# Optimization experiments

Measured on AMD Instinct MI355X. Metric: run time of the kernel, lower is better.

The kernel has to match this reference:

```python
import jax, jax.numpy as jnp
import numpy as np

DIM = 512
HID = 1024        # dim * expansion_factor
QK = 128          # query_key_dim
G = 256           # group_size
EPS = 1e-5


def setup_inputs() -> dict:
    key = jax.random.key(0)
    ks = jax.random.split(key, 6)
    x = jax.random.normal(ks[0], (4, 4096, DIM), jnp.float32)
    ln_w = jnp.ones((DIM,), jnp.float32)
    ln_b = jnp.zeros((DIM,), jnp.float32)
    Wh = 0.02 * jax.random.normal(ks[1], (DIM, 2 * HID), jnp.float32)
    bh = jnp.zeros((2 * HID,), jnp.float32)
    Wqk = 0.02 * jax.random.normal(ks[2], (DIM, QK), jnp.float32)
    bqk = jnp.zeros((QK,), jnp.float32)
    gamma = 0.02 * jax.random.normal(ks[3], (4, QK), jnp.float32)  # nn.init.normal_(gamma, std=0.02)
    beta = jnp.zeros((4, QK), jnp.float32)
    Wo = 0.02 * jax.random.normal(ks[4], (HID, DIM), jnp.float32)
    bo = jnp.zeros((DIM,), jnp.float32)
    return {"x": x, "ln_w": ln_w, "ln_b": ln_b, "Wh": Wh, "bh": bh,
            "Wqk": Wqk, "bqk": bqk, "gamma": gamma, "beta": beta,
            "Wo": Wo, "bo": bo}


def reference(x, ln_w, ln_b, Wh, bh, Wqk, bqk, gamma, beta, Wo, bo):
    b, n, _ = x.shape
    g = n // G  # number of groups (n chosen as multiple of G -> no padding)

    # LayerNorm (torch uses biased variance)
    mu = jnp.mean(x, axis=-1, keepdims=True)
    var = jnp.mean((x - mu) ** 2, axis=-1, keepdims=True)
    normed = (x - mu) * jax.lax.rsqrt(var + EPS) * ln_w + ln_b

    # to_hidden: Linear -> SiLU, split into v / gate
    h = jax.nn.silu(normed @ Wh + bh)            # [b, n, 2*HID]
    v, gate = jnp.split(h, 2, axis=-1)           # each [b, n, HID]

    # to_qk: Linear -> SiLU, then 4-head offset/scale
    qk = jax.nn.silu(normed @ Wqk + bqk)         # [b, n, QK]
    qkh = qk[..., None, :] * gamma + beta        # [b, n, 4, QK]
    quad_q, lin_q, quad_k, lin_k = (qkh[..., i, :] for i in range(4))

    # group: b (g n) d -> b g n d
    grp = lambda t: t.reshape(b, g, G, t.shape[-1])
    qq, qk_, lq, lk, vv = map(grp, (quad_q, quad_k, lin_q, lin_k, v))

    # quadratic (group-local) attention with ReLU^2 scores, causal within group
    sim = jnp.einsum('bgid,bgjd->bgij', qq, qk_) / G
    attn = jnp.square(jnp.maximum(sim, 0.0))
    causal_mask = jnp.triu(jnp.ones((G, G), dtype=bool), 1)
    attn = jnp.where(causal_mask, 0.0, attn)
    quad_out = jnp.einsum('bgij,bgje->bgie', attn, vv)   # [b, g, G, HID]

    # linear attention across groups: per-group kv, exclusive cumsum over group dim
    lin_kv = jnp.einsum('bgnd,bgne->bgde', lk, vv) / G   # [b, g, QK, HID]
    lin_kv = jnp.cumsum(lin_kv, axis=1)
    lin_kv = jnp.pad(lin_kv, ((0, 0), (1, 0), (0, 0), (0, 0)))[:, :-1]
    lin_out = jnp.einsum('bgde,bgnd->bgne', lin_kv, lq)  # [b, g, G, HID]

    out = gate * (quad_out.reshape(b, n, HID) + lin_out.reshape(b, n, HID))
    return out @ Wo + bo + x
```

## Files before the change

kernel.cpp:

```cpp
#include <hip/hip_runtime.h>
#include <hip/hip_bf16.h>
#include <math.h>


#define BATCH 4
#define SEQ   4096
#define TROWS 16384
#define DIMD  512
#define HIDD  1024
#define QKD   128
#define GRP   256
#define NGRP  16
#define BGRP  64
#define EPIW  132
#define EPB   130

typedef unsigned short bfraw;
typedef __attribute__((ext_vector_type(8))) short bf16x8;
typedef __attribute__((ext_vector_type(8))) unsigned short u16x8;
typedef __attribute__((ext_vector_type(4))) unsigned int u32x4;
typedef __attribute__((ext_vector_type(4))) float f32x4;

__device__ __forceinline__ float bf2f(bfraw u) {
    union { float f; unsigned int i; } c;
    c.i = ((unsigned int)u) << 16;
    return c.f;
}
__device__ __forceinline__ bfraw f2bf(float f) {
    unsigned int x = __float_as_uint(f);
    unsigned int r = (x + 0x7fffu + ((x >> 16) & 1u)) >> 16;
    return (bfraw)r;
}
__device__ __forceinline__ unsigned int pkbf(float lo, float hi) {
    __hip_bfloat162 h2 = __float22bfloat162_rn(make_float2(lo, hi));
    union { __hip_bfloat162 h; unsigned int u; } c; c.h = h2;
    return c.u;
}
__device__ __forceinline__ void store16bf(bfraw* dst, const float* src) {
    u32x4 a, b;
    #pragma unroll
    for (int k = 0; k < 4; ++k) a[k] = pkbf(src[2 * k], src[2 * k + 1]);
    #pragma unroll
    for (int k = 0; k < 4; ++k) b[k] = pkbf(src[8 + 2 * k], src[8 + 2 * k + 1]);
    *(u32x4*)dst = a;
    *(u32x4*)(dst + 8) = b;
}
__device__ __forceinline__ float silu_f(float z) {
    return z / (1.f + __expf(-z));
}
__device__ __forceinline__ void gload_lds16(const void* g, void* l) {
    __builtin_amdgcn_global_load_lds(
        (const __attribute__((address_space(1))) unsigned int*)g,
        (__attribute__((address_space(3))) unsigned int*)l, 16, 0, 0);
}

__device__ __forceinline__ void mfma_step(const bfraw* As, const bfraw* Bs,
                                          f32x4 acc[4][4], int wm, int wn,
                                          int q, int mi) {
    bf16x8 af[4], bfg[4];
    #pragma unroll
    for (int i = 0; i < 4; ++i)
        af[i] = *(const bf16x8*)&As[(size_t)(wm * 64 + i * 16 + mi) * 32 + q * 8];
    #pragma unroll
    for (int j = 0; j < 4; ++j)
        bfg[j] = *(const bf16x8*)&Bs[(size_t)(wn * 64 + j * 16 + mi) * 32 + q * 8];
    #pragma unroll
    for (int i = 0; i < 4; ++i)
        #pragma unroll
        for (int j = 0; j < 4; ++j)
            acc[i][j] = __builtin_amdgcn_mfma_f32_16x16x32_bf16(af[i], bfg[j], acc[i][j], 0, 0, 0);
}

#define SMEM_DECL(sz)                                           \
    __shared__ __align__(16) char smem_[sz];                    \
    bfraw* As0 = (bfraw*)smem_;                                 \
    bfraw* As1 = (bfraw*)(smem_ + 8192);                        \
    bfraw* Bs0 = (bfraw*)(smem_ + 16384);                       \
    bfraw* Bs1 = (bfraw*)(smem_ + 24576);

#define KLOOP_PRE(Abase, Astr, Bbase, Bstr)                                    \
    const bfraw* pa0 = (Abase) + (size_t)(t >> 2) * (Astr) + (t & 3) * 8;      \
    const bfraw* pa1 = pa0 + (size_t)64 * (Astr);                              \
    const bfraw* pb0 = (Bbase) + (size_t)(t >> 2) * (Bstr) + (t & 3) * 8;      \
    const bfraw* pb1 = pb0 + (size_t)64 * (Bstr);

#define LDS_DSTS                                                               \
    bfraw* lA0  = As0 + (size_t)wid * 512;                                     \
    bfraw* lA0b = As0 + 2048 + (size_t)wid * 512;                              \
    bfraw* lA1  = As1 + (size_t)wid * 512;                                     \
    bfraw* lA1b = As1 + 2048 + (size_t)wid * 512;                              \
    bfraw* lB0  = Bs0 + (size_t)wid * 512;                                     \
    bfraw* lB0b = Bs0 + 2048 + (size_t)wid * 512;                              \
    bfraw* lB1  = Bs1 + (size_t)wid * 512;                                     \
    bfraw* lB1b = Bs1 + 2048 + (size_t)wid * 512;

#define KSTEP64P                                                               \
    do {                                                                       \
        gload_lds16(pa0,      lA0);                                            \
        gload_lds16(pa1,      lA0b);                                           \
        gload_lds16(pa0 + 32, lA1);                                            \
        gload_lds16(pa1 + 32, lA1b);                                           \
        gload_lds16(pb0,      lB0);                                            \
        gload_lds16(pb1,      lB0b);                                           \
        gload_lds16(pb0 + 32, lB1);                                            \
        gload_lds16(pb1 + 32, lB1b);                                           \
        __syncthreads();                                                       \
        mfma_step(As0, Bs0, acc, wm, wn, q, mi);                               \
        mfma_step(As1, Bs1, acc, wm, wn, q, mi);                               \
        __syncthreads();                                                       \
        pa0 += 64; pa1 += 64; pb0 += 64; pb1 += 64;                            \
    } while (0)

__device__ __forceinline__ int epi_row(int p, int lr) {
    return (lr < 16) ? (p * 16 + lr) : (64 + p * 16 + (lr - 16));
}

__global__ __launch_bounds__(256) void prep_kernel(const float* __restrict__ x,
                                                   const float* __restrict__ lnw,
                                                   const float* __restrict__ lnb,
                                                   const float* __restrict__ Wh,
                                                   const float* __restrict__ Wo,
                                                   const float* __restrict__ Wqk,
                                                   bfraw* __restrict__ normb,
                                                   bfraw* __restrict__ WhT,
                                                   bfraw* __restrict__ WoT,
                                                   bfraw* __restrict__ WqkT) {
    __shared__ float tile[32][33];
    int bid = blockIdx.x;
    int t = threadIdx.x;
    if (bid < 4096) {
        int row  = bid * 4 + (t >> 6);
        int lane = t & 63;
        const float* xr = x + (size_t)row * DIMD;
        float4 v0 = ((const float4*)xr)[lane];
        float4 v1 = ((const float4*)xr)[lane + 64];
        float s  = v0.x + v0.y + v0.z + v0.w + v1.x + v1.y + v1.z + v1.w;
        float ss = v0.x*v0.x + v0.y*v0.y + v0.z*v0.z + v0.w*v0.w
                 + v1.x*v1.x + v1.y*v1.y + v1.z*v1.z + v1.w*v1.w;
        #pragma unroll
        for (int off = 32; off; off >>= 1) {
            s  += __shfl_xor(s, off);
            ss += __shfl_xor(ss, off);
        }
        float mu  = s * (1.f / DIMD);
        float var = ss * (1.f / DIMD) - mu * mu;
        float inv = rsqrtf(var + 1e-5f);
        float4 w0 = ((const float4*)lnw)[lane],  w1 = ((const float4*)lnw)[lane + 64];
        float4 b0 = ((const float4*)lnb)[lane],  b1 = ((const float4*)lnb)[lane + 64];
        unsigned int o0 = pkbf((v0.x - mu) * inv * w0.x + b0.x,
                               (v0.y - mu) * inv * w0.y + b0.y);
        unsigned int o1 = pkbf((v0.z - mu) * inv * w0.z + b0.z,
                               (v0.w - mu) * inv * w0.w + b0.w);
        unsigned int o2 = pkbf((v1.x - mu) * inv * w1.x + b1.x,
                               (v1.y - mu) * inv * w1.y + b1.y);
        unsigned int o3 = pkbf((v1.z - mu) * inv * w1.z + b1.z,
                               (v1.w - mu) * inv * w1.w + b1.w);
        unsigned int* brow = (unsigned int*)(normb + (size_t)row * DIMD);
        ((uint2*)brow)[lane]      = make_uint2(o0, o1);
        ((uint2*)brow)[lane + 64] = make_uint2(o2, o3);
        return;
    }
    bid -= 4096;
    const float* in; bfraw* outp; int R, C, nx;
    if (bid < 1024)      { in = Wh;  outp = WhT;  R = DIMD; C = 2 * HIDD; nx = 64; }
    else if (bid < 1536) { bid -= 1024; in = Wo;  outp = WoT;  R = HIDD; C = DIMD; nx = 16; }
    else                 { bid -= 1536; in = Wqk; outp = WqkT; R = DIMD; C = QKD;  nx = 4; }
    int c0 = (bid % nx) * 32, r0 = (bid / nx) * 32;
    int tr = t >> 3, tc4 = (t & 7) * 4;
    float4 v = *(const float4*)&in[(size_t)(r0 + tr) * C + c0 + tc4];
    tile[tr][tc4 + 0] = v.x; tile[tr][tc4 + 1] = v.y;
    tile[tr][tc4 + 2] = v.z; tile[tr][tc4 + 3] = v.w;
    __syncthreads();
    ushort4 s;
    s.x = f2bf(tile[tc4 + 0][tr]);
    s.y = f2bf(tile[tc4 + 1][tr]);
    s.z = f2bf(tile[tc4 + 2][tr]);
    s.w = f2bf(tile[tc4 + 3][tr]);
    *(ushort4*)&outp[(size_t)(c0 + tr) * R + r0 + tc4] = s;
}

__global__ __launch_bounds__(256) void gemm_h(const bfraw* __restrict__ A,
                                              const bfraw* __restrict__ WhT,
                                              const bfraw* __restrict__ WqkT,
                                              const float* __restrict__ bias,
                                              const float* __restrict__ bqk,
                                              const float* __restrict__ gamma,
                                              const float* __restrict__ beta,
                                              bfraw* __restrict__ vT,
                                              bfraw* __restrict__ gate,
                                              bfraw* __restrict__ qq,
                                              bfraw* __restrict__ lq,
                                              bfraw* __restrict__ kk,
                                              bfraw* __restrict__ lkT) {
    SMEM_DECL(33280)
    bfraw* epi2 = (bfraw*)smem_;
    float* epi = (float*)smem_;
    int t = threadIdx.x;
    int lane = t & 63, wid = t >> 6;
    int wm = wid >> 1, wn = wid & 1;
    int q = lane >> 4, mi = lane & 15;
    int row0 = blockIdx.y * 128, col0 = blockIdx.x * 128;
    bool is_qk = (blockIdx.x == 16);
    f32x4 acc[4][4] = {};
    LDS_DSTS
    {
        const bfraw* Bbase = is_qk ? WqkT : (WhT + (size_t)col0 * DIMD);
        KLOOP_PRE(A + (size_t)row0 * DIMD, DIMD, Bbase, DIMD)
        #pragma unroll
        for (int k0 = 0; k0 < DIMD; k0 += 64) KSTEP64P;
    }
    int bg = row0 >> 8;
    if (is_qk) {
        #pragma unroll
        for (int p = 0; p < 4; ++p) {
            #pragma unroll
            for (int j = 0; j < 4; ++j) {
                float bv = bqk[wn * 64 + j * 16 + mi];
                #pragma unroll
                for (int rg = 0; rg < 4; ++rg)
                    epi[(wm * 16 + q * 4 + rg) * EPIW + wn * 64 + j * 16 + mi] =
                        silu_f(acc[p][j][rg] + bv);
            }
            __syncthreads();
            {
                int lr = t >> 3, c0t = (t & 7) * 16;
                int gr = row0 + epi_row(p, lr);
                const float* src = &epi[lr * EPIW + c0t];
                float z[16];
                #pragma unroll
                for (int k = 0; k < 16; ++k) z[k] = src[k];
                #pragma unroll
                for (int hd = 0; hd < 3; ++hd) {
                    bfraw* arr = (hd == 0) ? qq : (hd == 1) ? lq : kk;
                    const float* gp = gamma + hd * QKD + c0t;
                    const float* ep = beta  + hd * QKD + c0t;
                    float tmp[16];
                    #pragma unroll
                    for (int k = 0; k < 16; ++k) tmp[k] = z[k] * gp[k] + ep[k];
                    store16bf(arr + (size_t)gr * QKD + c0t, tmp);
                }
            }
            {
                int c = t >> 1, half = t & 1;
                float g3 = gamma[3 * QKD + c], e3 = beta[3 * QKD + c];
                int j0 = (row0 & 255) + half * 64 + p * 16;
                float tmp[16];
                #pragma unroll
                for (int k = 0; k < 16; ++k)
                    tmp[k] = epi[(half * 16 + k) * EPIW + c] * g3 + e3;
                store16bf(lkT + ((size_t)bg * QKD + c) * GRP + j0, tmp);
            }
            __syncthreads();
        }
        return;
    }
    #pragma unroll
    for (int p = 0; p < 4; ++p)
        #pragma unroll
        for (int j = 0; j < 4; ++j) {
            float bv = bias[col0 + wn * 64 + j * 16 + mi];
            #pragma unroll
            for (int rg = 0; rg < 4; ++rg) {
                int rowl = wm * 64 + p * 16 + q * 4 + rg;
                epi2[rowl * EPB + wn * 64 + j * 16 + mi] = f2bf(silu_f(acc[p][j][rg] + bv));
            }
        }
    __syncthreads();
    if (col0 < HIDD) {
        int e2 = t & 63, jblk = t >> 6;
        const unsigned int* ep32 = (const unsigned int*)epi2;
        unsigned int wv[32];
        #pragma unroll
        for (int jj = 0; jj < 32; ++jj)
            wv[jj] = ep32[(size_t)(jblk * 32 + jj) * 65 + e2];
        int jbase = (row0 & 255) + jblk * 32;
        bfraw* dst0 = vT + ((size_t)bg * HIDD + col0 + 2 * e2) * GRP + jbase;
        bfraw* dst1 = dst0 + GRP;
        #pragma unroll
        for (int vq = 0; vq < 4; ++vq) {
            u16x8 s;
            #pragma unroll
            for (int k = 0; k < 8; ++k) s[k] = (bfraw)(wv[vq * 8 + k] & 0xffffu);
            *(u16x8*)(dst0 + vq * 8) = s;
        }
        #pragma unroll
        for (int vq = 0; vq < 4; ++vq) {
            u16x8 s;
            #pragma unroll
            for (int k = 0; k < 8; ++k) s[k] = (bfraw)(wv[vq * 8 + k] >> 16);
            *(u16x8*)(dst1 + vq * 8) = s;
        }
    } else {
        int lr = t >> 1, seg = t & 1;
        const bfraw* src = epi2 + (size_t)lr * EPB + seg * 64;
        bfraw* dst = gate + (size_t)(row0 + lr) * HIDD + (col0 - HIDD) + seg * 64;
        #pragma unroll
        for (int vq = 0; vq < 8; ++vq)
            *(u16x8*)(dst + vq * 8) = *(const u16x8*)(src + vq * 8);
    }
}

__global__ __launch_bounds__(256) void simkv_kernel(const bfraw* __restrict__ qq,
                                                    const bfraw* __restrict__ kk,
                                                    bfraw* __restrict__ attn,
                                                    const bfraw* __restrict__ vT,
                                                    const bfraw* __restrict__ lkT,
                                                    bfraw* __restrict__ kvT_raw) {
    SMEM_DECL(32768)
    float* epi = (float*)smem_;
    int t = threadIdx.x;
    int lane = t & 63, wid = t >> 6;
    int wm = wid >> 1, wn = wid & 1;
    int q = lane >> 4, mi = lane & 15;
    int bid = blockIdx.x;
    f32x4 acc[4][4] = {};
    LDS_DSTS
    if (bid < 512) {
        int bg = bid >> 3;
        int row0 = (bid & 7) * 128;
        {
            KLOOP_PRE(vT + (size_t)bg * HIDD * GRP + (size_t)row0 * GRP, GRP,
                      lkT + (size_t)bg * QKD * GRP, GRP)
            #pragma unroll
            for (int k0 = 0; k0 < GRP; k0 += 64) KSTEP64P;
        }
        bfraw* outg = kvT_raw + (size_t)bg * HIDD * QKD;
        #pragma unroll
        for (int p = 0; p < 4; ++p) {
            #pragma unroll
            for (int j = 0; j < 4; ++j)
                #pragma unroll
                for (int rg = 0; rg < 4; ++rg)
                    epi[(wm * 16 + q * 4 + rg) * EPIW + wn * 64 + j * 16 + mi] = acc[p][j][rg];
            __syncthreads();
            int lr = t >> 3, c0t = (t & 7) * 16;
            int gr = row0 + epi_row(p, lr);
            store16bf(outg + (size_t)gr * QKD + c0t, &epi[lr * EPIW + c0t]);
            __syncthreads();
        }
        return;
    }
    int i = bid - 512;
    int bg = i & 63;
    int tid = i >> 6;
    int ry = (tid == 0) ? 0 : 1;
    int rx = (tid == 2) ? 1 : 0;
    int row0 = ry * 128, col0 = rx * 128;
    {
        KLOOP_PRE(qq + (size_t)(bg * GRP + row0) * QKD, QKD,
                  kk + (size_t)(bg * GRP + col0) * QKD, QKD)
        #pragma unroll
        for (int k0 = 0; k0 < QKD; k0 += 64) KSTEP64P;
    }
    bfraw* ag = attn + (size_t)bg * GRP * GRP;
    #pragma unroll
    for (int p = 0; p < 4; ++p) {
        #pragma unroll
        for (int j = 0; j < 4; ++j) {
            int colg = col0 + wn * 64 + j * 16 + mi;
            #pragma unroll
            for (int rg = 0; rg < 4; ++rg) {
                int rowg = row0 + wm * 64 + p * 16 + q * 4 + rg;
                float s = acc[p][j][rg] * (1.f / GRP);
                s = fmaxf(s, 0.f);
                s = s * s;
                epi[(wm * 16 + q * 4 + rg) * EPIW + wn * 64 + j * 16 + mi] =
                    (colg > rowg) ? 0.f : s;
            }
        }
        __syncthreads();
        int lr = t >> 3, c0t = (t & 7) * 16;
        int gr = row0 + epi_row(p, lr);
        store16bf(ag + (size_t)gr * GRP + col0 + c0t, &epi[lr * EPIW + c0t]);
        __syncthreads();
    }
}

__global__ __launch_bounds__(256) void cumsum2_kernel(const bfraw* __restrict__ raw,
                                                      bfraw* __restrict__ ex) {
    int idx = blockIdx.x * 256 + threadIdx.x;
    int b = idx >> 17;
    int r = idx & 131071;
    const bfraw* rp = raw + (size_t)b * NGRP * 131072 + r;
    bfraw* ep = ex + (size_t)b * NGRP * 131072 + r;
    float run = 0.f;
    #pragma unroll
    for (int g = 0; g < NGRP; ++g) {
        ep[(size_t)g * 131072] = f2bf(run);
        run += bf2f(rp[(size_t)g * 131072]) * (1.f / GRP);
    }
}

__global__ __launch_bounds__(256) void quadlin_mfma(const bfraw* __restrict__ attn,
                                                    const bfraw* __restrict__ vT,
                                                    const bfraw* __restrict__ lq,
                                                    const bfraw* __restrict__ kvT_ex,
                                                    const bfraw* __restrict__ gate,
                                                    bfraw* __restrict__ gated) {
    int bg = blockIdx.z;
    int row0 = blockIdx.y * 128;
    int col0 = blockIdx.x * 128;
    SMEM_DECL(32768)
    float* epi = (float*)smem_;
    int t = threadIdx.x;
    int lane = t & 63, wid = t >> 6;
    int wm = wid >> 1, wn = wid & 1;
    int q = lane >> 4, mi = lane & 15;
    f32x4 acc[4][4] = {};
    LDS_DSTS
    {
        KLOOP_PRE(attn + (size_t)bg * GRP * GRP + (size_t)row0 * GRP, GRP,
                  vT + (size_t)bg * HIDD * GRP + (size_t)col0 * GRP, GRP)
        int kmax = row0 + 128;
        for (int k0 = 0; k0 < kmax; k0 += 64) KSTEP64P;
    }
    {
        KLOOP_PRE(lq + (size_t)(bg * GRP + row0) * QKD, QKD,
                  kvT_ex + (size_t)bg * HIDD * QKD + (size_t)col0 * QKD, QKD)
        #pragma unroll
        for (int k0 = 0; k0 < QKD; k0 += 64) KSTEP64P;
    }
    #pragma unroll
    for (int p = 0; p < 4; ++p) {
        #pragma unroll
        for (int j = 0; j < 4; ++j)
            #pragma unroll
            for (int rg = 0; rg < 4; ++rg)
                epi[(wm * 16 + q * 4 + rg) * EPIW + wn * 64 + j * 16 + mi] = acc[p][j][rg];
        __syncthreads();
        int lr = t >> 3, c0t = (t & 7) * 16;
        int gr = row0 + epi_row(p, lr);
        size_t grow = (size_t)bg * GRP + gr;
        const float* src = &epi[lr * EPIW + c0t];
        const bfraw* gsrc = gate + grow * HIDD + col0 + c0t;
        u16x8 g0 = *(const u16x8*)gsrc;
        u16x8 g1 = *(const u16x8*)(gsrc + 8);
        float tmp[16];
        #pragma unroll
        for (int k = 0; k < 8; ++k) tmp[k] = src[k] * bf2f(g0[k]);
        #pragma unroll
        for (int k = 0; k < 8; ++k) tmp[8 + k] = src[8 + k] * bf2f(g1[k]);
        store16bf(gated + grow * HIDD + col0 + c0t, tmp);
        __syncthreads();
    }
}

__global__ __launch_bounds__(256) void gemm_final(const bfraw* __restrict__ A,
                                                  const bfraw* __restrict__ BT,
                                                  const float* __restrict__ bo,
                                                  const float* __restrict__ x,
                                                  float* __restrict__ out) {
    SMEM_DECL(32768)
    float* epi = (float*)smem_;
    int t = threadIdx.x;
    int lane = t & 63, wid = t >> 6;
    int wm = wid >> 1, wn = wid & 1;
    int q = lane >> 4, mi = lane & 15;
    int row0 = blockIdx.y * 128, col0 = blockIdx.x * 128;
    f32x4 acc[4][4] = {};
    LDS_DSTS
    {
        KLOOP_PRE(A + (size_t)row0 * HIDD, HIDD, BT + (size_t)col0 * HIDD, HIDD)
        #pragma unroll
        for (int k0 = 0; k0 < HIDD; k0 += 64) KSTEP64P;
    }
    #pragma unroll
    for (int p = 0; p < 4; ++p) {
        #pragma unroll
        for (int j = 0; j < 4; ++j) {
            float bv = bo[col0 + wn * 64 + j * 16 + mi];
            #pragma unroll
            for (int rg = 0; rg < 4; ++rg)
                epi[(wm * 16 + q * 4 + rg) * EPIW + wn * 64 + j * 16 + mi] =
                    acc[p][j][rg] + bv;
        }
        __syncthreads();
        int lr = t >> 3, c0t = (t & 7) * 16;
        int gr = row0 + epi_row(p, lr);
        const float* src = &epi[lr * EPIW + c0t];
        const float* xsrc = x + (size_t)gr * DIMD + col0 + c0t;
        float* dst = out + (size_t)gr * DIMD + col0 + c0t;
        #pragma unroll
        for (int v = 0; v < 4; ++v) {
            float4 a = ((const float4*)src)[v];
            float4 xv = ((const float4*)xsrc)[v];
            a.x += xv.x; a.y += xv.y; a.z += xv.z; a.w += xv.w;
            ((float4*)dst)[v] = a;
        }
        __syncthreads();
    }
}

extern "C" void kernel_launch(void* const* d_in, const int* in_sizes, int n_in,
                              void* d_out, int out_size, void* d_ws, size_t ws_size,
                              hipStream_t stream) {
    const float* x     = (const float*)d_in[0];
    const float* ln_w  = (const float*)d_in[1];
    const float* ln_b  = (const float*)d_in[2];
    const float* Wh    = (const float*)d_in[3];
    const float* bh    = (const float*)d_in[4];
    const float* Wqk   = (const float*)d_in[5];
    const float* bqk   = (const float*)d_in[6];
    const float* gamma = (const float*)d_in[7];
    const float* beta  = (const float*)d_in[8];
    const float* Wo    = (const float*)d_in[9];
    const float* bo    = (const float*)d_in[10];
    float* out = (float*)d_out;

    char* outb_ = (char*)d_out;
    bfraw* attn = (bfraw*)(outb_);
    bfraw* qq   = (bfraw*)(outb_ + 8388608);
    bfraw* kk   = (bfraw*)(outb_ + 12582912);
    bfraw* lq   = (bfraw*)(outb_ + 16777216);
    bfraw* WhT  = (bfraw*)(outb_ + 20971520);
    bfraw* WqkT = (bfraw*)(outb_ + 23068672);

    char* wsb = (char*)d_ws;
    bfraw* vT      = (bfraw*)(wsb);
    bfraw* gate    = (bfraw*)(wsb + 33554432);
    bfraw* gated   = (bfraw*)(wsb + 67108864);
    bfraw* normb   = (bfraw*)(wsb + 100663296);
    bfraw* kvT_raw = (bfraw*)(wsb + 117440512);
    bfraw* kvT_ex  = (bfraw*)(wsb + 134217728);
    bfraw* lkT     = (bfraw*)(wsb + 150994944);
    bfraw* WoT     = (bfraw*)(wsb + 155189248);

    prep_kernel<<<4096 + 1024 + 512 + 64, 256, 0, stream>>>(
        x, ln_w, ln_b, Wh, Wo, Wqk, normb, WhT, WoT, WqkT);
    gemm_h<<<dim3(17, TROWS / 128), 256, 0, stream>>>(
        normb, WhT, WqkT, bh, bqk, gamma, beta, vT, gate, qq, lq, kk, lkT);
    simkv_kernel<<<512 + 192, 256, 0, stream>>>(qq, kk, attn, vT, lkT, kvT_raw);
    cumsum2_kernel<<<(BATCH * QKD * HIDD) / 256, 256, 0, stream>>>(kvT_raw, kvT_ex);
    quadlin_mfma<<<dim3(HIDD / 128, GRP / 128, BGRP), 256, 0, stream>>>(
        attn, vT, lq, kvT_ex, gate, gated);
    gemm_final<<<dim3(DIMD / 128, TROWS / 128), 256, 0, stream>>>(gated, WoT, bo, x, out);
}
```

Baseline: 282.6 us.

## Double-buffer LDS tiles so global loads overlap MFMA compute in all GEMMs

Replaces the load-all-then-compute K step with a two-stage ping-pong pipeline. The next 32-wide K slice is issued via global-to-LDS loads while MFMAs consume the current buffer. This hides global memory latency behind compute in every GEMM kernel. The catch is shallower K steps per barrier and possibly the same number of syncs per K, plus the risk that the loads were already partly hidden by occupancy.

```diff
diff --git a/kernel.cpp b/kernel.cpp
--- a/kernel.cpp
+++ b/kernel.cpp
@@ -71,12 +71,22 @@
             acc[i][j] = __builtin_amdgcn_mfma_f32_16x16x32_bf16(af[i], bfg[j], acc[i][j], 0, 0, 0);
 }
 
-#define SMEM_DECL(sz)                                           \
-    __shared__ __align__(16) char smem_[sz];                    \
-    bfraw* As0 = (bfraw*)smem_;                                 \
-    bfraw* As1 = (bfraw*)(smem_ + 8192);                        \
-    bfraw* Bs0 = (bfraw*)(smem_ + 16384);                       \
-    bfraw* Bs1 = (bfraw*)(smem_ + 24576);
+#define SMEMP_DECL                                              \
+    __shared__ __align__(16) char smem_[33280];                 \
+    bfraw* A0buf = (bfraw*)smem_;                               \
+    bfraw* B0buf = (bfraw*)(smem_ + 8192);                      \
+    bfraw* A1buf = (bfraw*)(smem_ + 16384);                     \
+    bfraw* B1buf = (bfraw*)(smem_ + 24576);
+
+#define PIPE_DSTS                                               \
+    bfraw* a0d  = A0buf + wid * 512;                            \
+    bfraw* a0d2 = A0buf + 2048 + wid * 512;                     \
+    bfraw* b0d  = B0buf + wid * 512;                            \
+    bfraw* b0d2 = B0buf + 2048 + wid * 512;                     \
+    bfraw* a1d  = A1buf + wid * 512;                            \
+    bfraw* a1d2 = A1buf + 2048 + wid * 512;                     \
+    bfraw* b1d  = B1buf + wid * 512;                            \
+    bfraw* b1d2 = B1buf + 2048 + wid * 512;
 
 #define KLOOP_PRE(Abase, Astr, Bbase, Bstr)                                    \
     const bfraw* pa0 = (Abase) + (size_t)(t >> 2) * (Astr) + (t & 3) * 8;      \
@@ -84,32 +94,30 @@
     const bfraw* pb0 = (Bbase) + (size_t)(t >> 2) * (Bstr) + (t & 3) * 8;      \
     const bfraw* pb1 = pb0 + (size_t)64 * (Bstr);
 
-#define LDS_DSTS                                                               \
-    bfraw* lA0  = As0 + (size_t)wid * 512;                                     \
-    bfraw* lA0b = As0 + 2048 + (size_t)wid * 512;                              \
-    bfraw* lA1  = As1 + (size_t)wid * 512;                                     \
-    bfraw* lA1b = As1 + 2048 + (size_t)wid * 512;                              \
-    bfraw* lB0  = Bs0 + (size_t)wid * 512;                                     \
-    bfraw* lB0b = Bs0 + 2048 + (size_t)wid * 512;                              \
-    bfraw* lB1  = Bs1 + (size_t)wid * 512;                                     \
-    bfraw* lB1b = Bs1 + 2048 + (size_t)wid * 512;
-
-#define KSTEP64P                                                               \
-    do {                                                                       \
-        gload_lds16(pa0,      lA0);                                            \
-        gload_lds16(pa1,      lA0b);                                           \
-        gload_lds16(pa0 + 32, lA1);                                            \
-        gload_lds16(pa1 + 32, lA1b);                                           \
-        gload_lds16(pb0,      lB0);                                            \
-        gload_lds16(pb1,      lB0b);                                           \
-        gload_lds16(pb0 + 32, lB1);                                            \
-        gload_lds16(pb1 + 32, lB1b);                                           \
+#define STAGE0                                                                 \
+    do { gload_lds16(pa0, a0d); gload_lds16(pa1, a0d2);                        \
+         gload_lds16(pb0, b0d); gload_lds16(pb1, b0d2);                        \
+         pa0 += 32; pa1 += 32; pb0 += 32; pb1 += 32; } while (0)
+#define STAGE1                                                                 \
+    do { gload_lds16(pa0, a1d); gload_lds16(pa1, a1d2);                        \
+         gload_lds16(pb0, b1d); gload_lds16(pb1, b1d2);                        \
+         pa0 += 32; pa1 += 32; pb0 += 32; pb1 += 32; } while (0)
+
+#define PIPE_LOOP(NIT, Abase, Astr, Bbase, Bstr)                               \
+    {                                                                          \
+        KLOOP_PRE(Abase, Astr, Bbase, Bstr)                                    \
+        STAGE0;                                                                \
+        for (int it = 0; it < (NIT); it += 2) {                                \
+            __syncthreads();                                                   \
+            if (it + 1 < (NIT)) STAGE1;                                        \
+            mfma_step(A0buf, B0buf, acc, wm, wn, q, mi);                       \
+            __syncthreads();                                                   \
+            if (it + 2 < (NIT)) STAGE0;                                        \
+            if (it + 1 < (NIT))                                                \
+                mfma_step(A1buf, B1buf, acc, wm, wn, q, mi);                   \
+        }                                                                      \
         __syncthreads();                                                       \
-        mfma_step(As0, Bs0, acc, wm, wn, q, mi);                               \
-        mfma_step(As1, Bs1, acc, wm, wn, q, mi);                               \
-        __syncthreads();                                                       \
-        pa0 += 64; pa1 += 64; pb0 += 64; pb1 += 64;                            \
-    } while (0)
+    }
 
 __device__ __forceinline__ int epi_row(int p, int lr) {
     return (lr < 16) ? (p * 16 + lr) : (64 + p * 16 + (lr - 16));
@@ -192,7 +200,7 @@
                                               bfraw* __restrict__ lq,
                                               bfraw* __restrict__ kk,
                                               bfraw* __restrict__ lkT) {
-    SMEM_DECL(33280)
+    SMEMP_DECL
     bfraw* epi2 = (bfraw*)smem_;
     float* epi = (float*)smem_;
     int t = threadIdx.x;
@@ -202,12 +210,10 @@
     int row0 = blockIdx.y * 128, col0 = blockIdx.x * 128;
     bool is_qk = (blockIdx.x == 16);
     f32x4 acc[4][4] = {};
-    LDS_DSTS
+    PIPE_DSTS
     {
         const bfraw* Bbase = is_qk ? WqkT : (WhT + (size_t)col0 * DIMD);
-        KLOOP_PRE(A + (size_t)row0 * DIMD, DIMD, Bbase, DIMD)
-        #pragma unroll
-        for (int k0 = 0; k0 < DIMD; k0 += 64) KSTEP64P;
+        PIPE_LOOP(16, A + (size_t)row0 * DIMD, DIMD, Bbase, DIMD)
     }
     int bg = row0 >> 8;
     if (is_qk) {
@@ -306,7 +312,7 @@
                                                     const bfraw* __restrict__ vT,
                                                     const bfraw* __restrict__ lkT,
                                                     bfraw* __restrict__ kvT_raw) {
-    SMEM_DECL(32768)
+    SMEMP_DECL
     float* epi = (float*)smem_;
     int t = threadIdx.x;
     int lane = t & 63, wid = t >> 6;
@@ -314,16 +320,12 @@
     int q = lane >> 4, mi = lane & 15;
     int bid = blockIdx.x;
     f32x4 acc[4][4] = {};
-    LDS_DSTS
+    PIPE_DSTS
     if (bid < 512) {
         int bg = bid >> 3;
         int row0 = (bid & 7) * 128;
-        {
-            KLOOP_PRE(vT + (size_t)bg * HIDD * GRP + (size_t)row0 * GRP, GRP,
-                      lkT + (size_t)bg * QKD * GRP, GRP)
-            #pragma unroll
-            for (int k0 = 0; k0 < GRP; k0 += 64) KSTEP64P;
-        }
+        PIPE_LOOP(8, vT + (size_t)bg * HIDD * GRP + (size_t)row0 * GRP, GRP,
+                  lkT + (size_t)bg * QKD * GRP, GRP)
         bfraw* outg = kvT_raw + (size_t)bg * HIDD * QKD;
         #pragma unroll
         for (int p = 0; p < 4; ++p) {
@@ -346,12 +348,8 @@
     int ry = (tid == 0) ? 0 : 1;
     int rx = (tid == 2) ? 1 : 0;
     int row0 = ry * 128, col0 = rx * 128;
-    {
-        KLOOP_PRE(qq + (size_t)(bg * GRP + row0) * QKD, QKD,
-                  kk + (size_t)(bg * GRP + col0) * QKD, QKD)
-        #pragma unroll
-        for (int k0 = 0; k0 < QKD; k0 += 64) KSTEP64P;
-    }
+    PIPE_LOOP(4, qq + (size_t)(bg * GRP + row0) * QKD, QKD,
+              kk + (size_t)(bg * GRP + col0) * QKD, QKD)
     bfraw* ag = attn + (size_t)bg * GRP * GRP;
     #pragma unroll
     for (int p = 0; p < 4; ++p) {
@@ -400,26 +398,21 @@
     int bg = blockIdx.z;
     int row0 = blockIdx.y * 128;
     int col0 = blockIdx.x * 128;
-    SMEM_DECL(32768)
+    SMEMP_DECL
     float* epi = (float*)smem_;
     int t = threadIdx.x;
     int lane = t & 63, wid = t >> 6;
     int wm = wid >> 1, wn = wid & 1;
     int q = lane >> 4, mi = lane & 15;
     f32x4 acc[4][4] = {};
-    LDS_DSTS
+    PIPE_DSTS
     {
-        KLOOP_PRE(attn + (size_t)bg * GRP * GRP + (size_t)row0 * GRP, GRP,
+        int nit = (row0 + 128) >> 5;
+        PIPE_LOOP(nit, attn + (size_t)bg * GRP * GRP + (size_t)row0 * GRP, GRP,
                   vT + (size_t)bg * HIDD * GRP + (size_t)col0 * GRP, GRP)
-        int kmax = row0 + 128;
-        for (int k0 = 0; k0 < kmax; k0 += 64) KSTEP64P;
-    }
-    {
-        KLOOP_PRE(lq + (size_t)(bg * GRP + row0) * QKD, QKD,
-                  kvT_ex + (size_t)bg * HIDD * QKD + (size_t)col0 * QKD, QKD)
-        #pragma unroll
-        for (int k0 = 0; k0 < QKD; k0 += 64) KSTEP64P;
-    }
+    }
+    PIPE_LOOP(4, lq + (size_t)(bg * GRP + row0) * QKD, QKD,
+              kvT_ex + (size_t)bg * HIDD * QKD + (size_t)col0 * QKD, QKD)
     #pragma unroll
     for (int p = 0; p < 4; ++p) {
         #pragma unroll
@@ -450,7 +443,7 @@
                                                   const float* __restrict__ bo,
                                                   const float* __restrict__ x,
                                                   float* __restrict__ out) {
-    SMEM_DECL(32768)
+    SMEMP_DECL
     float* epi = (float*)smem_;
     int t = threadIdx.x;
     int lane = t & 63, wid = t >> 6;
@@ -458,12 +451,8 @@
     int q = lane >> 4, mi = lane & 15;
     int row0 = blockIdx.y * 128, col0 = blockIdx.x * 128;
     f32x4 acc[4][4] = {};
-    LDS_DSTS
-    {
-        KLOOP_PRE(A + (size_t)row0 * HIDD, HIDD, BT + (size_t)col0 * HIDD, HIDD)
-        #pragma unroll
-        for (int k0 = 0; k0 < HIDD; k0 += 64) KSTEP64P;
-    }
+    PIPE_DSTS
+    PIPE_LOOP(32, A + (size_t)row0 * HIDD, HIDD, BT + (size_t)col0 * HIDD, HIDD)
     #pragma unroll
     for (int p = 0; p < 4; ++p) {
         #pragma unroll
```

After: 282.6 us. Within noise of the previous version (-0.0%).
